# Kernel tuning notes

Measured on AMD Instinct MI355X. Metric: run time of the kernel, lower is better.

Reference implementation:

```python
import jax, jax.numpy as jnp
import numpy as np
from jax import lax

H = 1024   # hidden_size
C = 64     # cond_size
L = 256    # latent_size
V = 32000  # num_of_word
NC = 8     # num_of_cond
T = 256    # MAX_LENGTH == seq len (teacher forcing, full length)


def setup_inputs() -> dict:
    key = jax.random.key(0)
    ks = jax.random.split(key, 26)
    p = lambda k, shape, s=0.05: (jax.random.normal(k, shape, jnp.float32) * s)
    inp = {
        # learned parameters
        "cond_emb": p(ks[0], (NC, C)),
        "enc_emb": p(ks[1], (V, H)),
        "enc_wih": p(ks[2], (4 * H, H)), "enc_whh": p(ks[3], (4 * H, H)),
        "enc_bih": p(ks[4], (4 * H,)), "enc_bhh": p(ks[5], (4 * H,)),
        "mean_w": p(ks[6], (L, H)), "mean_b": p(ks[7], (L,)),
        "lgv_w": p(ks[8], (L, H)), "lgv_b": p(ks[9], (L,)),
        "l2h_w": p(ks[10], (H, L + C)), "l2h_b": p(ks[11], (H,)),
        "l2c_w": p(ks[12], (H, L + C)), "l2c_b": p(ks[13], (H,)),
        "dec_emb": p(ks[14], (V, H)),
        "dec_wih": p(ks[15], (4 * H, H)), "dec_whh": p(ks[16], (4 * H, H)),
        "dec_bih": p(ks[17], (4 * H,)), "dec_bhh": p(ks[18], (4 * H,)),
        "out_w": p(ks[19], (V, H)), "out_b": p(ks[20], (V,)),
        # reparameterization noise (torch.normal in sample_z)
        "eps": jax.random.normal(ks[21], (L,), jnp.float32),
        # forward args
        "input_ids": jax.random.randint(ks[22], (T,), 0, V),
        "target_ids": jax.random.randint(ks[23], (T,), 0, V),
        "input_c": 2,
        "target_c": 3,
    }
    return inp


def _lstm_cell(h, c, x, wih, whh, bih, bhh):
    # torch LSTM gate order: i, f, g, o
    g = x @ wih.T + bih + h @ whh.T + bhh
    i, f, gg, o = jnp.split(g, 4)
    c = jax.nn.sigmoid(f) * c + jax.nn.sigmoid(i) * jnp.tanh(gg)
    h = jax.nn.sigmoid(o) * jnp.tanh(c)
    return h, c


def reference(cond_emb, enc_emb, enc_wih, enc_whh, enc_bih, enc_bhh,
              mean_w, mean_b, lgv_w, lgv_b, l2h_w, l2h_b, l2c_w, l2c_b,
              dec_emb, dec_wih, dec_whh, dec_bih, dec_bhh, out_w, out_b,
              eps, input_ids, target_ids, input_c, target_c):
    Hd = enc_whh.shape[1]
    cond_in = cond_emb[input_c]                              # (C,)
    # encoder initial hidden = cat(zeros(H-C), cond); cell = zeros(H)
    h0 = jnp.concatenate([jnp.zeros(Hd - cond_in.shape[0], cond_in.dtype), cond_in])
    c0 = jnp.zeros(Hd, cond_in.dtype)
    enc_x = enc_emb[input_ids]                               # (T, H)

    def enc_step(carry, x):
        h, c = _lstm_cell(carry[0], carry[1], x, enc_wih, enc_whh, enc_bih, enc_bhh)
        return (h, c), None
    (hT, _), _ = lax.scan(enc_step, (h0, c0), enc_x)

    m = mean_w @ hT + mean_b                                 # (L,)
    lgv = lgv_w @ hT + lgv_b                                 # (L,)
    z = eps * jnp.exp(lgv / 2) + m                           # reparameterize

    zc = jnp.concatenate([z, cond_emb[target_c]])            # (L+C,)
    dh0 = l2h_w @ zc + l2h_b
    dc0 = l2c_w @ zc + l2c_b

    # teacher forcing: decoder inputs = [SOS=0, target[:-1]], T steps
    dec_in = jnp.concatenate([jnp.zeros((1,), target_ids.dtype), target_ids[:-1]])
    dec_x = dec_emb[dec_in]                                  # (T, H)

    def dec_step(carry, x):
        h, c = _lstm_cell(carry[0], carry[1], x, dec_wih, dec_whh, dec_bih, dec_bhh)
        return (h, c), h
    _, hs = lax.scan(dec_step, (dh0, dc0), dec_x)            # (T, H)

    logits = hs @ out_w.T + out_b                            # (T, V)
    return logits, m, lgv
```

## Files before the change

### kernel.cpp

```cpp
#include <hip/hip_runtime.h>
#include <hip/hip_bf16.h>

#define HD   1024
#define G4   4096
#define CND  64
#define LAT  256
#define VOC  32000
#define TT   256
#define ZCN  320
#define NWG  64
#define THR  512
#define DEC0 301u

typedef unsigned long long u64;
typedef __attribute__((ext_vector_type(8))) short short8;
typedef __attribute__((ext_vector_type(4))) float f32x4;

__device__ __forceinline__ float sig_f(float x) {
    return 1.0f / (1.0f + __expf(-x));
}
__device__ __forceinline__ float tanh_f(float x) {
    float e = __expf(2.0f * x);
    return 1.0f - 2.0f / (e + 1.0f);
}

__device__ __forceinline__ u64 al64(const u64* p) {
    return __hip_atomic_load((u64*)p, __ATOMIC_RELAXED, __HIP_MEMORY_SCOPE_AGENT);
}
__device__ __forceinline__ void as64(u64* p, u64 v) {
    __hip_atomic_store(p, v, __ATOMIC_RELAXED, __HIP_MEMORY_SCOPE_AGENT);
}
__device__ __forceinline__ u64 packhv(float h, unsigned tag) {
    return ((u64)tag << 32) | (u64)__float_as_uint(h);
}

#define BM  128
#define BN  128
#define BK  32
#define LDT 40

__device__ __forceinline__ void cvt2(float x, ushort& h, ushort& l)
{
    unsigned u = __float_as_uint(x);
    h = (ushort)(u >> 16);
    float hif = __uint_as_float(u & 0xffff0000u);
    l = (ushort)(__float_as_uint(x - hif) >> 16);
}
__device__ __forceinline__ unsigned pk(ushort a, ushort b)
{
    return (unsigned)a | ((unsigned)b << 16);
}

__device__ __forceinline__ void stage16(const float* __restrict__ src,
                                        ushort* __restrict__ dh,
                                        ushort* __restrict__ dl)
{
    ushort h[16], l[16];
    #pragma unroll
    for (int i = 0; i < 16; i += 4) {
        float4 v = *(const float4*)(src + i);
        cvt2(v.x, h[i],   l[i]);
        cvt2(v.y, h[i+1], l[i+1]);
        cvt2(v.z, h[i+2], l[i+2]);
        cvt2(v.w, h[i+3], l[i+3]);
    }
    uint4 H0 = {pk(h[0],h[1]), pk(h[2],h[3]), pk(h[4],h[5]), pk(h[6],h[7])};
    uint4 H1 = {pk(h[8],h[9]), pk(h[10],h[11]), pk(h[12],h[13]), pk(h[14],h[15])};
    uint4 L0 = {pk(l[0],l[1]), pk(l[2],l[3]), pk(l[4],l[5]), pk(l[6],l[7])};
    uint4 L1 = {pk(l[8],l[9]), pk(l[10],l[11]), pk(l[12],l[13]), pk(l[14],l[15])};
    *(uint4*)(dh)     = H0;
    *(uint4*)(dh + 8) = H1;
    *(uint4*)(dl)     = L0;
    *(uint4*)(dl + 8) = L1;
}

__global__ __launch_bounds__(256) void k_gemm3(
    const float* __restrict__ A, const int* __restrict__ ids, int shift,
    const float* __restrict__ B, const float* __restrict__ bias1,
    const float* __restrict__ bias2, float* __restrict__ C,
    int ntn, int ldc)
{
    __shared__ ushort Ah[BM * LDT], Al[BM * LDT];
    __shared__ ushort Bh[BM * LDT], Bl[BM * LDT];

    const int bid  = blockIdx.x;
    const int m0   = (bid / ntn) * BM;
    const int n0   = (bid % ntn) * BN;
    const int tid  = threadIdx.x;
    const int lane = tid & 63;
    const int wid  = tid >> 6;
    const int wm   = (wid >> 1) * 64;
    const int wn   = (wid & 1) * 64;

    const int sr = tid >> 1;
    const int sc = (tid & 1) * 16;

    int ar = m0 + sr;
    if (ids) ar = shift ? ((ar == 0) ? 0 : ids[ar - 1]) : ids[ar];
    const float* arow = A + (size_t)ar * HD;
    const float* brow = B + (size_t)(n0 + sr) * HD;

    f32x4 acc[4][4] = {};

    const int fr = lane & 15;
    const int kg = (lane >> 4) * 8;

    for (int k0 = 0; k0 < HD; k0 += BK) {
        __syncthreads();
        stage16(arow + k0 + sc, &Ah[sr * LDT + sc], &Al[sr * LDT + sc]);
        stage16(brow + k0 + sc, &Bh[sr * LDT + sc], &Bl[sr * LDT + sc]);
        __syncthreads();

        short8 fah[4], fal[4], fbh[4], fbl[4];
        #pragma unroll
        for (int f = 0; f < 4; ++f) {
            fah[f] = *(const short8*)&Ah[(wm + f * 16 + fr) * LDT + kg];
            fal[f] = *(const short8*)&Al[(wm + f * 16 + fr) * LDT + kg];
            fbh[f] = *(const short8*)&Bh[(wn + f * 16 + fr) * LDT + kg];
            fbl[f] = *(const short8*)&Bl[(wn + f * 16 + fr) * LDT + kg];
        }
        #pragma unroll
        for (int fi = 0; fi < 4; ++fi)
            #pragma unroll
            for (int fj = 0; fj < 4; ++fj) {
                acc[fi][fj] = __builtin_amdgcn_mfma_f32_16x16x32_bf16(
                                  fah[fi], fbh[fj], acc[fi][fj], 0, 0, 0);
                acc[fi][fj] = __builtin_amdgcn_mfma_f32_16x16x32_bf16(
                                  fah[fi], fbl[fj], acc[fi][fj], 0, 0, 0);
                acc[fi][fj] = __builtin_amdgcn_mfma_f32_16x16x32_bf16(
                                  fal[fi], fbh[fj], acc[fi][fj], 0, 0, 0);
            }
    }

    const int rg = (lane >> 4) * 4;
    #pragma unroll
    for (int fj = 0; fj < 4; ++fj) {
        int col = n0 + wn + fj * 16 + fr;
        float bs = bias1[col];
        if (bias2) bs += bias2[col];
        #pragma unroll
        for (int fi = 0; fi < 4; ++fi) {
            #pragma unroll
            for (int r = 0; r < 4; ++r) {
                int rowi = m0 + wm + fi * 16 + rg + r;
                C[(size_t)rowi * ldc + col] = acc[fi][fj][r] + bs;
            }
        }
    }
}

#define WCH 132

__device__ __forceinline__ void load_w(float4 (&wreg)[32],
                                       const float* __restrict__ w,
                                       int row, int s)
{
    const float4* p = (const float4*)(w + (size_t)row * HD + s * 128);
    #pragma unroll
    for (int u = 0; u < 32; ++u) wreg[u] = p[u];
}

__device__ __forceinline__ void read_h(const u64* mb, unsigned v,
                                       float* h_lds, int tid)
{
    const u64* p = mb + (size_t)(v & 1u) * HD + tid * 2;
    u64 e0, e1;
    for (;;) {
        e0 = al64(p); e1 = al64(p + 1);
        if ((unsigned)(e0 >> 32) >= v && (unsigned)(e1 >> 32) >= v) break;
        __builtin_amdgcn_s_sleep(1);
    }
    int j = tid * 2;
    *(float2*)&h_lds[(j >> 7) * WCH + (j & 127)] =
        make_float2(__uint_as_float((unsigned)e0),
                    __uint_as_float((unsigned)e1));
}

__device__ __forceinline__ void lstm_loop(
    const float* __restrict__ pre, u64* mb, float* __restrict__ hs,
    float& c_reg, const float4 (&wreg)[32], float* h_lds, float* g_lds,
    int tid, int s, int rl, int row, int j_own, unsigned vbase)
{
    float pv = (s == 0) ? pre[row] : 0.f;
    for (int t = 0; t < TT; ++t) {
        unsigned v = vbase + (unsigned)t;
        float pv_nxt = 0.f;
        if (s == 0 && t + 1 < TT) pv_nxt = pre[(size_t)(t + 1) * G4 + row];

        read_h(mb, v, h_lds, tid);
        __syncthreads();

        const float4* h4 = (const float4*)h_lds;
        float a0 = 0.f, a1 = 0.f, a2 = 0.f, a3 = 0.f;
        #pragma unroll
        for (int u = 0; u < 32; ++u) {
            float4 wv = wreg[u];
            float4 hv = h4[s * 33 + u];
            a0 = fmaf(wv.x, hv.x, a0);
            a1 = fmaf(wv.y, hv.y, a1);
            a2 = fmaf(wv.z, hv.z, a2);
            a3 = fmaf(wv.w, hv.w, a3);
        }
        float acc = (a0 + a1) + (a2 + a3);
        acc += __shfl_xor(acc, 1);
        acc += __shfl_xor(acc, 2);
        acc += __shfl_xor(acc, 4);
        if (s == 0) g_lds[rl] = acc + pv;
        __syncthreads();

        if (tid < 64) {
            float g = g_lds[tid];
            float a = (tid >= 32 && tid < 48) ? tanh_f(g) : sig_f(g);
            float xf = __shfl(a, tid + 16);
            float xg = __shfl(a, tid + 32);
            float xo = __shfl(a, tid + 48);
            if (tid < 16) {
                c_reg = xf * c_reg + a * xg;
                float hv = xo * tanh_f(c_reg);
                as64(&mb[(size_t)((v + 1u) & 1u) * HD + j_own],
                     packhv(hv, v + 1u));
                if (hs) hs[(size_t)t * HD + j_own] = hv;
            }
        }
        pv = pv_nxt;
    }
}

__global__ __launch_bounds__(512, 1) void k_seq(
    const float* __restrict__ cond_emb, const float* __restrict__ enc_whh,
    const float* __restrict__ mean_w, const float* __restrict__ mean_b,
    const float* __restrict__ lgv_w, const float* __restrict__ lgv_b,
    const float* __restrict__ l2h_w, const float* __restrict__ l2h_b,
    const float* __restrict__ l2c_w, const float* __restrict__ l2c_b,
    const float* __restrict__ dec_whh, const float* __restrict__ eps,
    const int* __restrict__ p_ic, const int* __restrict__ p_tc,
    const float* __restrict__ pre_enc, const float* __restrict__ pre_dec,
    u64* mb, u64* zmb,
    float* __restrict__ hs, float* __restrict__ out_mlgv)
{
    __shared__ float h_lds[8 * WCH];
    __shared__ float g_lds[64];
    __shared__ float red[32];
    __shared__ float sm[8];

    const int w   = blockIdx.x;
    const int tid = threadIdx.x;
    const int s   = tid & 7;
    const int rl  = tid >> 3;
    const int gate = rl >> 4;
    const int jl   = rl & 15;
    const int row  = gate * HD + w * 16 + jl;
    const int j_own = w * 16 + tid;
    float c_reg = 0.f;

    if (tid < 16) {
        int j = j_own;
        float v0 = 0.f;
        int ic = p_ic[0];
        if (j >= HD - CND) v0 = cond_emb[ic * CND + (j - (HD - CND))];
        as64(&mb[(size_t)1 * HD + j], packhv(v0, 1u));
    }

    float4 wreg[32];
    load_w(wreg, enc_whh, row, s);
    lstm_loop(pre_enc, mb, nullptr, c_reg, wreg, h_lds, g_lds,
              tid, s, rl, row, j_own, 1u);

    read_h(mb, TT + 1u, h_lds, tid);
    __syncthreads();
    {
        int d = tid >> 6;
        int l64 = tid & 63;
        int l = w * 4 + (d & 3);
        const float* wrow = (d < 4 ? mean_w : lgv_w) + (size_t)l * HD;
        float acc = 0.f;
        #pragma unroll
        for (int e = 0; e < 16; ++e) {
            int k = e * 64 + l64;
            acc = fmaf(wrow[k], h_lds[(k >> 7) * WCH + (k & 127)], acc);
        }
        #pragma unroll
        for (int o = 32; o >= 1; o >>= 1) acc += __shfl_xor(acc, o);
        if (l64 == 0) sm[d] = acc + (d < 4 ? mean_b : lgv_b)[l];
    }
    __syncthreads();
    if (tid < 4) {
        int l = w * 4 + tid;
        float m = sm[tid], lg = sm[4 + tid];
        float z = eps[l] * __expf(0.5f * lg) + m;
        as64(&zmb[l], packhv(z, 1u));
        out_mlgv[l]       = m;
        out_mlgv[LAT + l] = lg;
    }

    if (tid < LAT) {
        u64 e;
        const u64* p = zmb + tid;
        do { e = al64(p); } while ((unsigned)(e >> 32) < 1u);
        h_lds[tid] = __uint_as_float((unsigned)e);
    } else if (tid < ZCN) {
        int tc = p_tc[0];
        h_lds[tid] = cond_emb[tc * CND + (tid - LAT)];
    }
    __syncthreads();
    {
        int r2 = tid >> 4;
        int l16 = tid & 15;
        int which = r2 >> 4;
        int i = w * 16 + (r2 & 15);
        const float* wrow = (which ? l2c_w : l2h_w) + (size_t)i * ZCN;
        float acc = 0.f;
        #pragma unroll
        for (int e = 0; e < 20; ++e) {
            int k = e * 16 + l16;
            acc = fmaf(wrow[k], h_lds[k], acc);
        }
        acc += __shfl_xor(acc, 1);
        acc += __shfl_xor(acc, 2);
        acc += __shfl_xor(acc, 4);
        acc += __shfl_xor(acc, 8);
        if (l16 == 0) red[r2] = acc + (which ? l2c_b : l2h_b)[i];
    }
    __syncthreads();
    if (tid < 16) {
        as64(&mb[(size_t)(DEC0 & 1u) * HD + j_own], packhv(red[tid], DEC0));
        c_reg = red[16 + tid];
    }

    load_w(wreg, dec_whh, row, s);
    lstm_loop(pre_dec, mb, hs, c_reg, wreg, h_lds, g_lds,
              tid, s, rl, row, j_own, DEC0);
}

extern "C" void kernel_launch(void* const* d_in, const int* in_sizes, int n_in,
                              void* d_out, int out_size, void* d_ws, size_t ws_size,
                              hipStream_t stream)
{
    const float* cond_emb = (const float*)d_in[0];
    const float* enc_emb  = (const float*)d_in[1];
    const float* enc_wih  = (const float*)d_in[2];
    const float* enc_whh  = (const float*)d_in[3];
    const float* enc_bih  = (const float*)d_in[4];
    const float* enc_bhh  = (const float*)d_in[5];
    const float* mean_w   = (const float*)d_in[6];
    const float* mean_b   = (const float*)d_in[7];
    const float* lgv_w    = (const float*)d_in[8];
    const float* lgv_b    = (const float*)d_in[9];
    const float* l2h_w    = (const float*)d_in[10];
    const float* l2h_b    = (const float*)d_in[11];
    const float* l2c_w    = (const float*)d_in[12];
    const float* l2c_b    = (const float*)d_in[13];
    const float* dec_emb  = (const float*)d_in[14];
    const float* dec_wih  = (const float*)d_in[15];
    const float* dec_whh  = (const float*)d_in[16];
    const float* dec_bih  = (const float*)d_in[17];
    const float* dec_bhh  = (const float*)d_in[18];
    const float* out_w    = (const float*)d_in[19];
    const float* out_b    = (const float*)d_in[20];
    const float* eps      = (const float*)d_in[21];
    const int* input_ids  = (const int*)d_in[22];
    const int* target_ids = (const int*)d_in[23];
    const int* p_ic       = (const int*)d_in[24];
    const int* p_tc       = (const int*)d_in[25];

    float* ws      = (float*)d_ws;
    float* pre_enc = ws;
    float* pre_dec = pre_enc + (size_t)TT * G4;
    float* hs      = pre_dec + (size_t)TT * G4;
    u64*   mb      = (u64*)(hs + (size_t)TT * HD);
    u64*   zmb     = mb + 2 * HD;

    float* outp     = (float*)d_out;
    float* out_mlgv = outp + (size_t)TT * VOC;

    const int* no_ids = nullptr;
    const float* no_bias = nullptr;

    hipMemsetAsync(mb, 0, (2 * HD + LAT) * sizeof(u64), stream);

    hipLaunchKernelGGL(k_gemm3, dim3(2 * 32), dim3(256), 0, stream,
                       enc_emb, input_ids, 0, enc_wih, enc_bih, enc_bhh,
                       pre_enc, 32, G4);
    hipLaunchKernelGGL(k_gemm3, dim3(2 * 32), dim3(256), 0, stream,
                       dec_emb, target_ids, 1, dec_wih, dec_bih, dec_bhh,
                       pre_dec, 32, G4);

    void* args[] = {
        (void*)&cond_emb, (void*)&enc_whh, (void*)&mean_w, (void*)&mean_b,
        (void*)&lgv_w, (void*)&lgv_b, (void*)&l2h_w, (void*)&l2h_b,
        (void*)&l2c_w, (void*)&l2c_b, (void*)&dec_whh, (void*)&eps,
        (void*)&p_ic, (void*)&p_tc, (void*)&pre_enc, (void*)&pre_dec,
        (void*)&mb, (void*)&zmb, (void*)&hs, (void*)&out_mlgv
    };
    hipLaunchCooperativeKernel((const void*)k_seq, dim3(NWG), dim3(THR),
                               args, 0, stream);

    hipLaunchKernelGGL(k_gemm3, dim3(2 * 250), dim3(256), 0, stream,
                       hs, no_ids, 0, out_w, out_b, no_bias,
                       outp, 250, VOC);
}
```

Baseline: 1.216 ms.

## Fuse input GEMMs, LSTM recurrence and output projection into one persistent kernel

```diff
diff --git a/kernel.cpp b/kernel.cpp
--- a/kernel.cpp
+++ b/kernel.cpp
@@ -8,9 +8,12 @@
 #define VOC  32000
 #define TT   256
 #define ZCN  320
-#define NWG  64
+#define NSEQ 64
+#define NWKR 160
 #define THR  512
 #define DEC0 301u
+#define WCH  132
+#define LDT  40
 
 typedef unsigned long long u64;
 typedef __attribute__((ext_vector_type(8))) short short8;
@@ -23,7 +26,6 @@
     float e = __expf(2.0f * x);
     return 1.0f - 2.0f / (e + 1.0f);
 }
-
 __device__ __forceinline__ u64 al64(const u64* p) {
     return __hip_atomic_load((u64*)p, __ATOMIC_RELAXED, __HIP_MEMORY_SCOPE_AGENT);
 }
@@ -33,11 +35,9 @@
 __device__ __forceinline__ u64 packhv(float h, unsigned tag) {
     return ((u64)tag << 32) | (u64)__float_as_uint(h);
 }
-
-#define BM  128
-#define BN  128
-#define BK  32
-#define LDT 40
+__device__ __forceinline__ float lo_f(u64 e) {
+    return __uint_as_float((unsigned)e);
+}
 
 __device__ __forceinline__ void cvt2(float x, ushort& h, ushort& l)
 {
@@ -50,7 +50,6 @@
 {
     return (unsigned)a | ((unsigned)b << 16);
 }
-
 __device__ __forceinline__ void stage16(const float* __restrict__ src,
                                         ushort* __restrict__ dh,
                                         ushort* __restrict__ dl)
@@ -64,65 +63,79 @@
         cvt2(v.z, h[i+2], l[i+2]);
         cvt2(v.w, h[i+3], l[i+3]);
     }
-    uint4 H0 = {pk(h[0],h[1]), pk(h[2],h[3]), pk(h[4],h[5]), pk(h[6],h[7])};
-    uint4 H1 = {pk(h[8],h[9]), pk(h[10],h[11]), pk(h[12],h[13]), pk(h[14],h[15])};
-    uint4 L0 = {pk(l[0],l[1]), pk(l[2],l[3]), pk(l[4],l[5]), pk(l[6],l[7])};
-    uint4 L1 = {pk(l[8],l[9]), pk(l[10],l[11]), pk(l[12],l[13]), pk(l[14],l[15])};
-    *(uint4*)(dh)     = H0;
-    *(uint4*)(dh + 8) = H1;
-    *(uint4*)(dl)     = L0;
-    *(uint4*)(dl + 8) = L1;
-}
-
-__global__ __launch_bounds__(256) void k_gemm3(
-    const float* __restrict__ A, const int* __restrict__ ids, int shift,
-    const float* __restrict__ B, const float* __restrict__ bias1,
-    const float* __restrict__ bias2, float* __restrict__ C,
-    int ntn, int ldc)
-{
-    __shared__ ushort Ah[BM * LDT], Al[BM * LDT];
-    __shared__ ushort Bh[BM * LDT], Bl[BM * LDT];
-
-    const int bid  = blockIdx.x;
-    const int m0   = (bid / ntn) * BM;
-    const int n0   = (bid % ntn) * BN;
-    const int tid  = threadIdx.x;
-    const int lane = tid & 63;
-    const int wid  = tid >> 6;
-    const int wm   = (wid >> 1) * 64;
-    const int wn   = (wid & 1) * 64;
-
-    const int sr = tid >> 1;
-    const int sc = (tid & 1) * 16;
-
-    int ar = m0 + sr;
-    if (ids) ar = shift ? ((ar == 0) ? 0 : ids[ar - 1]) : ids[ar];
-    const float* arow = A + (size_t)ar * HD;
-    const float* brow = B + (size_t)(n0 + sr) * HD;
-
-    f32x4 acc[4][4] = {};
-
-    const int fr = lane & 15;
-    const int kg = (lane >> 4) * 8;
-
-    for (int k0 = 0; k0 < HD; k0 += BK) {
+    *(uint4*)(dh)     = uint4{pk(h[0],h[1]),pk(h[2],h[3]),pk(h[4],h[5]),pk(h[6],h[7])};
+    *(uint4*)(dh + 8) = uint4{pk(h[8],h[9]),pk(h[10],h[11]),pk(h[12],h[13]),pk(h[14],h[15])};
+    *(uint4*)(dl)     = uint4{pk(l[0],l[1]),pk(l[2],l[3]),pk(l[4],l[5]),pk(l[6],l[7])};
+    *(uint4*)(dl + 8) = uint4{pk(l[8],l[9]),pk(l[10],l[11]),pk(l[12],l[13]),pk(l[14],l[15])};
+}
+
+__device__ void gemm64(int mode, int m0, int n0,
+    const float* __restrict__ A, const int* __restrict__ ids,
+    const u64* __restrict__ Amb,
+    const float* __restrict__ B, const float* __restrict__ b1,
+    const float* __restrict__ b2,
+    float* __restrict__ C, u64* __restrict__ Cmb, int ldc,
+    ushort* Ah, ushort* Al, ushort* Bh, ushort* Bl, int* idsb, int tid)
+{
+    if (mode != 2 && tid < 64) {
+        int m = m0 + tid;
+        idsb[tid] = (mode == 1) ? ((m == 0) ? 0 : ids[m - 1]) : ids[m];
+    }
+    __syncthreads();
+
+    const int lane = tid & 63, wid = tid >> 6;
+    const int wn  = wid * 32;
+    const int sr  = tid >> 3, sc  = (tid & 7) * 4;
+    const int sr2 = tid >> 1, sc2 = (tid & 1) * 16;
+    const int fr = lane & 15, kg = (lane >> 4) * 8, rg = (lane >> 4) * 4;
+
+    const float* brow = B + (size_t)(n0 + sr2) * HD;
+
+    f32x4 acc[4][2] = {};
+
+    for (int k0 = 0; k0 < HD; k0 += 32) {
         __syncthreads();
-        stage16(arow + k0 + sc, &Ah[sr * LDT + sc], &Al[sr * LDT + sc]);
-        stage16(brow + k0 + sc, &Bh[sr * LDT + sc], &Bl[sr * LDT + sc]);
+        {
+            float av[4];
+            if (mode == 2) {
+                const u64* ap = Amb + (size_t)(m0 + sr) * HD + k0 + sc;
+                #pragma unroll
+                for (int i = 0; i < 4; ++i) {
+                    u64 e = al64(ap + i);
+                    while ((unsigned)(e >> 32) == 0u) {
+                        __builtin_amdgcn_s_sleep(1);
+                        e = al64(ap + i);
+                    }
+                    av[i] = lo_f(e);
+                }
+            } else {
+                float4 v = *(const float4*)(A + (size_t)idsb[sr] * HD + k0 + sc);
+                av[0] = v.x; av[1] = v.y; av[2] = v.z; av[3] = v.w;
+            }
+            ushort h4[4], l4[4];
+            #pragma unroll
+            for (int i = 0; i < 4; ++i) cvt2(av[i], h4[i], l4[i]);
+            *(uint2*)&Ah[sr * LDT + sc] = uint2{pk(h4[0],h4[1]), pk(h4[2],h4[3])};
+            *(uint2*)&Al[sr * LDT + sc] = uint2{pk(l4[0],l4[1]), pk(l4[2],l4[3])};
+        }
+        stage16(brow + k0 + sc2, &Bh[sr2 * LDT + sc2], &Bl[sr2 * LDT + sc2]);
         __syncthreads();
 
-        short8 fah[4], fal[4], fbh[4], fbl[4];
+        short8 fah[4], fal[4], fbh[2], fbl[2];
         #pragma unroll
         for (int f = 0; f < 4; ++f) {
-            fah[f] = *(const short8*)&Ah[(wm + f * 16 + fr) * LDT + kg];
-            fal[f] = *(const short8*)&Al[(wm + f * 16 + fr) * LDT + kg];
+            fah[f] = *(const short8*)&Ah[(f * 16 + fr) * LDT + kg];
+            fal[f] = *(const short8*)&Al[(f * 16 + fr) * LDT + kg];
+        }
+        #pragma unroll
+        for (int f = 0; f < 2; ++f) {
             fbh[f] = *(const short8*)&Bh[(wn + f * 16 + fr) * LDT + kg];
             fbl[f] = *(const short8*)&Bl[(wn + f * 16 + fr) * LDT + kg];
         }
         #pragma unroll
         for (int fi = 0; fi < 4; ++fi)
             #pragma unroll
-            for (int fj = 0; fj < 4; ++fj) {
+            for (int fj = 0; fj < 2; ++fj) {
                 acc[fi][fj] = __builtin_amdgcn_mfma_f32_16x16x32_bf16(
                                   fah[fi], fbh[fj], acc[fi][fj], 0, 0, 0);
                 acc[fi][fj] = __builtin_amdgcn_mfma_f32_16x16x32_bf16(
@@ -132,24 +145,23 @@
             }
     }
 
-    const int rg = (lane >> 4) * 4;
     #pragma unroll
-    for (int fj = 0; fj < 4; ++fj) {
+    for (int fj = 0; fj < 2; ++fj) {
         int col = n0 + wn + fj * 16 + fr;
-        float bs = bias1[col];
-        if (bias2) bs += bias2[col];
+        float bs = b1[col];
+        if (b2) bs += b2[col];
         #pragma unroll
         for (int fi = 0; fi < 4; ++fi) {
             #pragma unroll
             for (int r = 0; r < 4; ++r) {
-                int rowi = m0 + wm + fi * 16 + rg + r;
-                C[(size_t)rowi * ldc + col] = acc[fi][fj][r] + bs;
+                int rowi = m0 + fi * 16 + rg + r;
+                float val = acc[fi][fj][r] + bs;
+                if (mode == 2) C[(size_t)rowi * ldc + col] = val;
+                else           as64(&Cmb[(size_t)rowi * ldc + col], packhv(val, 1u));
             }
         }
     }
 }
-
-#define WCH 132
 
 __device__ __forceinline__ void load_w(float4 (&wreg)[32],
                                        const float* __restrict__ w,
@@ -172,20 +184,31 @@
     }
     int j = tid * 2;
     *(float2*)&h_lds[(j >> 7) * WCH + (j & 127)] =
-        make_float2(__uint_as_float((unsigned)e0),
-                    __uint_as_float((unsigned)e1));
+        make_float2(lo_f(e0), lo_f(e1));
 }
 
 __device__ __forceinline__ void lstm_loop(
-    const float* __restrict__ pre, u64* mb, float* __restrict__ hs,
-    float& c_reg, const float4 (&wreg)[32], float* h_lds, float* g_lds,
-    int tid, int s, int rl, int row, int j_own, unsigned vbase)
-{
-    float pv = (s == 0) ? pre[row] : 0.f;
+    const u64* __restrict__ pre, u64* mb, u64* hs_mb,
+    float& c_reg, const float4 (&wreg)[32], float* h_lds,
+    int tid, int s, int gate, int row, int jown, int own, unsigned vbase)
+{
+    const int lane = tid & 63;
+    u64 pe = 0;
+    if (s == 0) pe = al64(pre + row);
     for (int t = 0; t < TT; ++t) {
         unsigned v = vbase + (unsigned)t;
-        float pv_nxt = 0.f;
-        if (s == 0 && t + 1 < TT) pv_nxt = pre[(size_t)(t + 1) * G4 + row];
+        __syncthreads();
+
+        float pv = 0.f;
+        if (s == 0) {
+            const u64* pp = pre + (size_t)t * G4 + row;
+            while ((unsigned)(pe >> 32) == 0u) {
+                __builtin_amdgcn_s_sleep(1);
+                pe = al64(pp);
+            }
+            pv = lo_f(pe);
+            if (t + 1 < TT) pe = al64(pp + G4);
+        }
 
         read_h(mb, v, h_lds, tid);
         __syncthreads();
@@ -205,56 +228,44 @@
         acc += __shfl_xor(acc, 1);
         acc += __shfl_xor(acc, 2);
         acc += __shfl_xor(acc, 4);
-        if (s == 0) g_lds[rl] = acc + pv;
-        __syncthreads();
-
-        if (tid < 64) {
-            float g = g_lds[tid];
-            float a = (tid >= 32 && tid < 48) ? tanh_f(g) : sig_f(g);
-            float xf = __shfl(a, tid + 16);
-            float xg = __shfl(a, tid + 32);
-            float xo = __shfl(a, tid + 48);
-            if (tid < 16) {
-                c_reg = xf * c_reg + a * xg;
-                float hv = xo * tanh_f(c_reg);
-                as64(&mb[(size_t)((v + 1u) & 1u) * HD + j_own],
-                     packhv(hv, v + 1u));
-                if (hs) hs[(size_t)t * HD + j_own] = hv;
-            }
-        }
-        pv = pv_nxt;
-    }
-}
-
-__global__ __launch_bounds__(512, 1) void k_seq(
-    const float* __restrict__ cond_emb, const float* __restrict__ enc_whh,
-    const float* __restrict__ mean_w, const float* __restrict__ mean_b,
-    const float* __restrict__ lgv_w, const float* __restrict__ lgv_b,
-    const float* __restrict__ l2h_w, const float* __restrict__ l2h_b,
-    const float* __restrict__ l2c_w, const float* __restrict__ l2c_b,
-    const float* __restrict__ dec_whh, const float* __restrict__ eps,
-    const int* __restrict__ p_ic, const int* __restrict__ p_tc,
-    const float* __restrict__ pre_enc, const float* __restrict__ pre_dec,
-    u64* mb, u64* zmb,
-    float* __restrict__ hs, float* __restrict__ out_mlgv)
-{
-    __shared__ float h_lds[8 * WCH];
-    __shared__ float g_lds[64];
-    __shared__ float red[32];
-    __shared__ float sm[8];
-
-    const int w   = blockIdx.x;
-    const int tid = threadIdx.x;
-    const int s   = tid & 7;
-    const int rl  = tid >> 3;
-    const int gate = rl >> 4;
-    const int jl   = rl & 15;
+
+        float x = acc + pv;
+        float a = (gate == 2) ? tanh_f(x) : sig_f(x);
+        float xf = __shfl(a, lane + 8);
+        float xg = __shfl(a, lane + 16);
+        float xo = __shfl(a, lane + 24);
+        if (own) {
+            c_reg = xf * c_reg + a * xg;
+            float hv2 = xo * tanh_f(c_reg);
+            as64(&mb[(size_t)((v + 1u) & 1u) * HD + jown], packhv(hv2, v + 1u));
+            if (hs_mb) as64(&hs_mb[(size_t)t * HD + jown], packhv(hv2, 1u));
+        }
+    }
+}
+
+__device__ void seq_role(
+    const float* cond_emb, const float* enc_whh,
+    const float* mean_w, const float* mean_b,
+    const float* lgv_w, const float* lgv_b,
+    const float* l2h_w, const float* l2h_b,
+    const float* l2c_w, const float* l2c_b,
+    const float* dec_whh, const float* eps,
+    const int* p_ic, const int* p_tc,
+    const u64* pre_enc, const u64* pre_dec,
+    u64* mb, u64* zmb, u64* hs_mb, float* out_mlgv,
+    float* h_lds, float* red_s, float* sm_s, int w, int tid)
+{
+    const int s    = tid & 7;
+    const int rl   = tid >> 3;
+    const int gate = rl & 3;
+    const int jl   = rl >> 2;
     const int row  = gate * HD + w * 16 + jl;
-    const int j_own = w * 16 + tid;
+    const int own  = ((tid & 31) == 0);
+    const int jown = w * 16 + (tid >> 5);
     float c_reg = 0.f;
 
     if (tid < 16) {
-        int j = j_own;
+        int j = w * 16 + tid;
         float v0 = 0.f;
         int ic = p_ic[0];
         if (j >= HD - CND) v0 = cond_emb[ic * CND + (j - (HD - CND))];
@@ -263,9 +274,10 @@
 
     float4 wreg[32];
     load_w(wreg, enc_whh, row, s);
-    lstm_loop(pre_enc, mb, nullptr, c_reg, wreg, h_lds, g_lds,
-              tid, s, rl, row, j_own, 1u);
-
+    lstm_loop(pre_enc, mb, nullptr, c_reg, wreg, h_lds,
+              tid, s, gate, row, jown, own, 1u);
+
+    __syncthreads();
     read_h(mb, TT + 1u, h_lds, tid);
     __syncthreads();
     {
@@ -281,12 +293,12 @@
         }
         #pragma unroll
         for (int o = 32; o >= 1; o >>= 1) acc += __shfl_xor(acc, o);
-        if (l64 == 0) sm[d] = acc + (d < 4 ? mean_b : lgv_b)[l];
+        if (l64 == 0) sm_s[d] = acc + (d < 4 ? mean_b : lgv_b)[l];
     }
     __syncthreads();
     if (tid < 4) {
         int l = w * 4 + tid;
-        float m = sm[tid], lg = sm[4 + tid];
+        float m = sm_s[tid], lg = sm_s[4 + tid];
         float z = eps[l] * __expf(0.5f * lg) + m;
         as64(&zmb[l], packhv(z, 1u));
         out_mlgv[l]       = m;
@@ -297,7 +309,7 @@
         u64 e;
         const u64* p = zmb + tid;
         do { e = al64(p); } while ((unsigned)(e >> 32) < 1u);
-        h_lds[tid] = __uint_as_float((unsigned)e);
+        h_lds[tid] = lo_f(e);
     } else if (tid < ZCN) {
         int tc = p_tc[0];
         h_lds[tid] = cond_emb[tc * CND + (tid - LAT)];
@@ -319,17 +331,87 @@
         acc += __shfl_xor(acc, 2);
         acc += __shfl_xor(acc, 4);
         acc += __shfl_xor(acc, 8);
-        if (l16 == 0) red[r2] = acc + (which ? l2c_b : l2h_b)[i];
-    }
-    __syncthreads();
-    if (tid < 16) {
-        as64(&mb[(size_t)(DEC0 & 1u) * HD + j_own], packhv(red[tid], DEC0));
-        c_reg = red[16 + tid];
-    }
+        if (l16 == 0) red_s[r2] = acc + (which ? l2c_b : l2h_b)[i];
+    }
+    __syncthreads();
+    if (tid < 16)
+        as64(&mb[(size_t)1 * HD + w * 16 + tid], packhv(red_s[tid], DEC0));
+    if (own) c_reg = red_s[16 + (tid >> 5)];
 
     load_w(wreg, dec_whh, row, s);
-    lstm_loop(pre_dec, mb, hs, c_reg, wreg, h_lds, g_lds,
-              tid, s, rl, row, j_own, DEC0);
+    lstm_loop(pre_dec, mb, hs_mb, c_reg, wreg, h_lds,
+              tid, s, gate, row, jown, own, DEC0);
+}
+
+__device__ void worker_role(int k,
+    const float* enc_emb, const int* input_ids,
+    const float* enc_wih, const float* enc_bih, const float* enc_bhh,
+    const float* dec_emb, const int* target_ids,
+    const float* dec_wih, const float* dec_bih, const float* dec_bhh,
+    const float* out_w, const float* out_b,
+    u64* pre_enc, u64* pre_dec, const u64* hs_mb, float* outp,
+    ushort* Ah, ushort* Al, ushort* Bh, ushort* Bl, int* idsb, int tid)
+{
+    if (k < 128) {
+        int dir = k >> 6, idx = k & 63;
+        int m0 = (idx >> 4) * 64, n0 = (idx & 15) * 256;
+        if (dir == 0)
+            gemm64(0, m0, n0, enc_emb, input_ids, nullptr, enc_wih,
+                   enc_bih, enc_bhh, nullptr, pre_enc, G4,
+                   Ah, Al, Bh, Bl, idsb, tid);
+        else
+            gemm64(1, m0, n0, dec_emb, target_ids, nullptr, dec_wih,
+                   dec_bih, dec_bhh, nullptr, pre_dec, G4,
+                   Ah, Al, Bh, Bl, idsb, tid);
+    }
+    for (int j = k; j < 500; j += NWKR) {
+        int m0 = (j / 125) * 64, n0 = (j % 125) * 256;
+        gemm64(2, m0, n0, nullptr, nullptr, hs_mb, out_w, out_b, nullptr,
+               outp, nullptr, VOC, Ah, Al, Bh, Bl, idsb, tid);
+    }
+}
+
+__global__ __launch_bounds__(THR, 2) void k_fused(
+    const float* cond_emb, const float* enc_emb,
+    const float* enc_wih, const float* enc_whh,
+    const float* enc_bih, const float* enc_bhh,
+    const float* mean_w, const float* mean_b,
+    const float* lgv_w, const float* lgv_b,
+    const float* l2h_w, const float* l2h_b,
+    const float* l2c_w, const float* l2c_b,
+    const float* dec_emb, const float* dec_wih, const float* dec_whh,
+    const float* dec_bih, const float* dec_bhh,
+    const float* out_w, const float* out_b, const float* eps,
+    const int* input_ids, const int* target_ids,
+    const int* p_ic, const int* p_tc,
+    u64* pre_mb, u64* hs_mb, u64* mb, u64* zmb,
+    float* outp, float* out_mlgv)
+{
+    __shared__ float  h_lds[8 * WCH];
+    __shared__ float  red_s[32];
+    __shared__ float  sm_s[8];
+    __shared__ ushort AhS[64 * LDT];
+    __shared__ ushort AlS[64 * LDT];
+    __shared__ ushort BhS[256 * LDT];
+    __shared__ ushort BlS[256 * LDT];
+    __shared__ int    idsb_s[64];
+
+    const int wg  = blockIdx.x;
+    const int tid = threadIdx.x;
+    u64* pre_enc = pre_mb;
+    u64* pre_dec = pre_mb + (size_t)TT * G4;
+
+    if (wg < NSEQ) {
+        seq_role(cond_emb, enc_whh, mean_w, mean_b, lgv_w, lgv_b,
+                 l2h_w, l2h_b, l2c_w, l2c_b, dec_whh, eps, p_ic, p_tc,
+                 pre_enc, pre_dec, mb, zmb, hs_mb, out_mlgv,
+                 h_lds, red_s, sm_s, wg, tid);
+    } else {
+        worker_role(wg - NSEQ, enc_emb, input_ids, enc_wih, enc_bih, enc_bhh,
+                    dec_emb, target_ids, dec_wih, dec_bih, dec_bhh,
+                    out_w, out_b, pre_enc, pre_dec, hs_mb, outp,
+                    AhS, AlS, BhS, BlS, idsb_s, tid);
+    }
 }
 
 extern "C" void kernel_launch(void* const* d_in, const int* in_sizes, int n_in,
@@ -363,39 +445,28 @@
     const int* p_ic       = (const int*)d_in[24];
     const int* p_tc       = (const int*)d_in[25];
 
-    float* ws      = (float*)d_ws;
-    float* pre_enc = ws;
-    float* pre_dec = pre_enc + (size_t)TT * G4;
-    float* hs      = pre_dec + (size_t)TT * G4;
-    u64*   mb      = (u64*)(hs + (size_t)TT * HD);
-    u64*   zmb     = mb + 2 * HD;
+    u64* pre_mb = (u64*)d_ws;
+    u64* hs_mb  = pre_mb + (size_t)2 * TT * G4;
+    u64* mb     = hs_mb + (size_t)TT * HD;
+    u64* zmb    = mb + 2 * HD;
 
     float* outp     = (float*)d_out;
     float* out_mlgv = outp + (size_t)TT * VOC;
 
-    const int* no_ids = nullptr;
-    const float* no_bias = nullptr;
-
-    hipMemsetAsync(mb, 0, (2 * HD + LAT) * sizeof(u64), stream);
-
-    hipLaunchKernelGGL(k_gemm3, dim3(2 * 32), dim3(256), 0, stream,
-                       enc_emb, input_ids, 0, enc_wih, enc_bih, enc_bhh,
-                       pre_enc, 32, G4);
-    hipLaunchKernelGGL(k_gemm3, dim3(2 * 32), dim3(256), 0, stream,
-                       dec_emb, target_ids, 1, dec_wih, dec_bih, dec_bhh,
-                       pre_dec, 32, G4);
+    size_t mb_total = ((size_t)2 * TT * G4 + (size_t)TT * HD + 2 * HD + LAT)
+                      * sizeof(u64);
+    hipMemsetAsync(pre_mb, 0, mb_total, stream);
 
     void* args[] = {
-        (void*)&cond_emb, (void*)&enc_whh, (void*)&mean_w, (void*)&mean_b,
+        (void*)&cond_emb, (void*)&enc_emb, (void*)&enc_wih, (void*)&enc_whh,
+        (void*)&enc_bih, (void*)&enc_bhh, (void*)&mean_w, (void*)&mean_b,
         (void*)&lgv_w, (void*)&lgv_b, (void*)&l2h_w, (void*)&l2h_b,
-        (void*)&l2c_w, (void*)&l2c_b, (void*)&dec_whh, (void*)&eps,
-        (void*)&p_ic, (void*)&p_tc, (void*)&pre_enc, (void*)&pre_dec,
-        (void*)&mb, (void*)&zmb, (void*)&hs, (void*)&out_mlgv
+        (void*)&l2c_w, (void*)&l2c_b, (void*)&dec_emb, (void*)&dec_wih,
+        (void*)&dec_whh, (void*)&dec_bih, (void*)&dec_bhh, (void*)&out_w,
+        (void*)&out_b, (void*)&eps, (void*)&input_ids, (void*)&target_ids,
+        (void*)&p_ic, (void*)&p_tc, (void*)&pre_mb, (void*)&hs_mb,
+        (void*)&mb, (void*)&zmb, (void*)&outp, (void*)&out_mlgv
     };
-    hipLaunchCooperativeKernel((const void*)k_seq, dim3(NWG), dim3(THR),
-                               args, 0, stream);
-
-    hipLaunchKernelGGL(k_gemm3, dim3(2 * 250), dim3(256), 0, stream,
-                       hs, no_ids, 0, out_w, out_b, no_bias,
-                       outp, 250, VOC);
-}
+    hipLaunchCooperativeKernel((const void*)k_fused, dim3(NSEQ + NWKR),
+                               dim3(THR), args, 0, stream);
+}
```

After: 1.287 ms. 1.06x slower.
